# Performance work log

Hardware: AMD Instinct MI355X
Metric: run time of the kernel (lower is better)

## Reference

```python
import jax, jax.numpy as jnp
import numpy as np

E, K = 16, 4          # n_experts, top_k
C, H = 2048, 3584     # d_model, ffn_hidden
B, T = 2, 512
STD = 0.02


def setup_inputs() -> dict:
    key = jax.random.key(0)
    ks = jax.random.split(key, 5)
    x = jax.random.normal(ks[0], (B, T, C), jnp.float32)
    W_up = jax.random.normal(ks[1], (E, H, C), jnp.float32) * STD
    W_gate = jax.random.normal(ks[2], (E, H, C), jnp.float32) * STD
    W_down = jax.random.normal(ks[3], (E, C, H), jnp.float32) * STD
    gate_inp = jax.random.normal(ks[4], (E, C), jnp.float32) * STD
    return {"x": x, "W_up": W_up, "W_gate": W_gate, "W_down": W_down,
            "gate_inp": gate_inp}


def reference(x, W_up, W_gate, W_down, gate_inp):
    # x: [B, T, C]
    b, t, c = x.shape
    xf = x.reshape(b * t, c)                                  # [N, C]
    logits = xf @ gate_inp.T                                  # [N, E]
    topv, topi = jax.lax.top_k(logits, K)                     # [N, K]
    w = jax.nn.softmax(topv.astype(jnp.float32), axis=-1).astype(x.dtype)
    n = xf.shape[0]
    # Dense combine weights: zero for unselected experts -> identical math
    # to the original per-token gather, without the [N,K,H,C] blowup.
    dense_w = jnp.zeros((n, E), x.dtype).at[jnp.arange(n)[:, None], topi].set(w)
    u = jnp.einsum('nc,ehc->neh', xf, W_up)                   # [N, E, H]
    g = jnp.einsum('nc,ehc->neh', xf, W_gate)                 # [N, E, H]
    h = jax.nn.silu(g) * u                                    # SwiGLU
    y = jnp.einsum('neh,ech,ne->nc', h, W_down, dense_w)      # weighted combine
    return y.reshape(b, t, c)
```

## Files before the change

### kernel.cpp

```cpp
#include <hip/hip_runtime.h>
#include <math.h>

#define NTOK   1024
#define EXP    16
#define TOPK   4
#define DMODEL 2048
#define DFFN   3584
#define HT_TILES 56
#define CT_TILES 32
#define NSLOT  4096
#define MCH    128
#define NCHMAX 48

typedef __attribute__((ext_vector_type(8))) short bf16x8;
typedef __attribute__((ext_vector_type(4))) float f32x4;

#define O_COUNTS 0
#define O_BASE   256
#define O_CURSOR 512
#define O_CHT    1024
#define O_TOPI   4096
#define O_TOPW   (O_TOPI + 16384)
#define O_TOK    (O_TOPW + 16384)
#define O_WGT    (O_TOK + 16384)
#define O_SLOTNK (O_WGT + 16384)
#define O_XG     (O_SLOTNK + 16384)
#define O_HBUF   (O_XG + (size_t)NSLOT*DMODEL*2)

#define VMW(N) asm volatile("s_waitcnt vmcnt(" #N ")" ::: "memory")
#define LKW0() asm volatile("s_waitcnt lgkmcnt(0)" ::: "memory")
#define BAR()  __builtin_amdgcn_s_barrier()

__device__ __forceinline__ unsigned short f2b_rne(float f) {
  unsigned u = __builtin_bit_cast(unsigned, f);
  u += 0x7FFFu + ((u >> 16) & 1u);
  return (unsigned short)(u >> 16);
}
__device__ __forceinline__ float b2f(unsigned short h) {
  unsigned u = ((unsigned)h) << 16;
  return __builtin_bit_cast(float, u);
}
__device__ __forceinline__ unsigned pk2(float lo, float hi) {
  unsigned r;
  asm("v_cvt_pk_bf16_f32 %0, %1, %2" : "=v"(r) : "v"(lo), "v"(hi));
  return r;
}
__device__ __forceinline__ bf16x8 pack8(float4 a, float4 b) {
  union { unsigned u[4]; bf16x8 v; } r;
  r.u[0] = pk2(a.x, a.y); r.u[1] = pk2(a.z, a.w);
  r.u[2] = pk2(b.x, b.y); r.u[3] = pk2(b.z, b.w);
  return r.v;
}

__device__ __forceinline__ void gl16(const unsigned short* g, unsigned short* l) {
  __builtin_amdgcn_global_load_lds(
      (const __attribute__((address_space(1))) void*)g,
      (__attribute__((address_space(3))) void*)l, 16, 0, 0);
}

__device__ __forceinline__ bf16x8 ld_frag(const unsigned short* lds, int row, int chunk) {
  return *(const bf16x8*)(lds + row*64 + ((chunk ^ (row & 7)) * 8));
}

__global__ void k_zero(int* counts, int* cursor) {
  int t = threadIdx.x;
  if (t < EXP) { counts[t] = 0; cursor[t] = 0; }
}

__global__ void k_gate(const float* __restrict__ x, const float* __restrict__ gi,
                       int* __restrict__ topi, float* __restrict__ topw,
                       int* __restrict__ counts) {
  int n = blockIdx.x;
  int lane = threadIdx.x & 63, wave = threadIdx.x >> 6;
  __shared__ float lg[EXP];
  const float4* xr = (const float4*)(x + (size_t)n * DMODEL);
  #pragma unroll
  for (int i = 0; i < 4; ++i) {
    int e = wave * 4 + i;
    const float4* gr = (const float4*)(gi + (size_t)e * DMODEL);
    float s = 0.f;
    #pragma unroll
    for (int j = 0; j < 8; ++j) {
      float4 a = xr[j*64 + lane];
      float4 b = gr[j*64 + lane];
      s += a.x*b.x + a.y*b.y + a.z*b.z + a.w*b.w;
    }
    #pragma unroll
    for (int off = 32; off; off >>= 1) s += __shfl_xor(s, off);
    if (lane == 0) lg[e] = s;
  }
  __syncthreads();
  if (threadIdx.x == 0) {
    float v[EXP];
    #pragma unroll
    for (int j = 0; j < EXP; ++j) v[j] = lg[j];
    int bi[TOPK]; float bv[TOPK];
    #pragma unroll
    for (int k = 0; k < TOPK; ++k) {
      float best = -3.4e38f; int bidx = 0;
      for (int j = 0; j < EXP; ++j) if (v[j] > best) { best = v[j]; bidx = j; }
      bv[k] = best; bi[k] = bidx; v[bidx] = -3.4e38f;
    }
    float m = bv[0], ss = 0.f, w[TOPK];
    #pragma unroll
    for (int k = 0; k < TOPK; ++k) { w[k] = expf(bv[k] - m); ss += w[k]; }
    #pragma unroll
    for (int k = 0; k < TOPK; ++k) {
      topi[n*TOPK + k] = bi[k];
      topw[n*TOPK + k] = w[k] / ss;
      atomicAdd(&counts[bi[k]], 1);
    }
  }
}

__global__ void k_prefix(const int* __restrict__ counts, int* __restrict__ basep,
                         int* __restrict__ chtab) {
  if (threadIdx.x == 0) {
    int acc = 0;
    for (int e = 0; e < EXP; ++e) { basep[e] = acc; acc += counts[e]; }
    int c = 0;
    for (int e = 0; e < EXP; ++e) {
      int nm = (counts[e] + MCH - 1) / MCH;
      for (int m = 0; m < nm; ++m) { chtab[1 + c] = (e << 8) | m; ++c; }
    }
    chtab[0] = c;
    for (; c < NCHMAX; ++c) chtab[1 + c] = -1;
  }
}

__global__ void k_scatter(const int* __restrict__ topi, const float* __restrict__ topw,
                          const int* __restrict__ basep, int* __restrict__ cursor,
                          int* __restrict__ tok, float* __restrict__ wgt,
                          int* __restrict__ slotnk) {
  int n = blockIdx.x * blockDim.x + threadIdx.x;
  if (n >= NTOK) return;
  #pragma unroll
  for (int k = 0; k < TOPK; ++k) {
    int e = topi[n*TOPK + k];
    int pos = atomicAdd(&cursor[e], 1);
    int slot = basep[e] + pos;
    tok[slot] = n;
    wgt[slot] = topw[n*TOPK + k];
    slotnk[n*TOPK + k] = slot;
  }
}

__global__ void k_gather(const float* __restrict__ x, const int* __restrict__ tok,
                         unsigned short* __restrict__ xg) {
  int slot = blockIdx.x;
  int t = tok[slot];
  int c0 = threadIdx.x * 8;
  const float* src = x + (size_t)t * DMODEL + c0;
  float4 a = *(const float4*)(src);
  float4 b = *(const float4*)(src + 4);
  uint4 o = {pk2(a.x, a.y), pk2(a.z, a.w), pk2(b.x, b.y), pk2(b.z, b.w)};
  *(uint4*)(xg + (size_t)slot * DMODEL + c0) = o;
}

#define UG_STEP(PC, PN, KC, CUR) do {                                          \
    VMW(12);                                                                   \
    BAR();                                                                     \
    VMW(4);                                                                    \
    PN[0] = pack8(rw0, rw1); PN[1] = pack8(rw2, rw3);                          \
    PN[2] = pack8(rw4, rw5); PN[3] = pack8(rw6, rw7);                          \
    int kn_ = (KC) + 2; if (kn_ > DMODEL/64 - 1) kn_ = DMODEL/64 - 1;          \
    const float* pu_ = wu_row + kn_*64;                                        \
    const float* pg_ = wg_row + kn_*64;                                        \
    rw0 = *(const float4*)(pu_);      rw1 = *(const float4*)(pu_ + 4);         \
    rw2 = *(const float4*)(pu_ + 32); rw3 = *(const float4*)(pu_ + 36);        \
    rw4 = *(const float4*)(pg_);      rw5 = *(const float4*)(pg_ + 4);         \
    rw6 = *(const float4*)(pg_ + 32); rw7 = *(const float4*)(pg_ + 36);        \
    int wb_ = (CUR) + 2; if (wb_ >= 3) wb_ -= 3;                               \
    unsigned short* xw_ = xs + wb_*8192;                                       \
    _Pragma("unroll")                                                          \
    for (int i_ = 0; i_ < 4; ++i_)                                             \
      gl16(bx[i_] + kn_*64, xw_ + (i_*4 + wave)*8*64);                         \
    const unsigned short* xr_ = xs + (CUR)*8192;                               \
    __builtin_amdgcn_s_setprio(1);                                             \
    _Pragma("unroll")                                                          \
    for (int kk_ = 0; kk_ < 2; ++kk_) {                                        \
      int chunk_ = kk_*4 + (lane >> 4);                                        \
      _Pragma("unroll")                                                        \
      for (int t_ = 0; t_ < 8; ++t_) {                                         \
        bf16x8 a_ = ld_frag(xr_, t_*16 + col, chunk_);                         \
        ua[t_] = __builtin_amdgcn_mfma_f32_16x16x32_bf16(a_, PC[kk_],   ua[t_], 0, 0, 0); \
        ga[t_] = __builtin_amdgcn_mfma_f32_16x16x32_bf16(a_, PC[2+kk_], ga[t_], 0, 0, 0); \
      }                                                                        \
    }                                                                          \
    __builtin_amdgcn_s_setprio(0);                                             \
  } while (0)

__global__ __launch_bounds__(256, 3) void k_upgate(
    const unsigned short* __restrict__ xg,
    const float* __restrict__ Wu, const float* __restrict__ Wg,
    const int* __restrict__ counts, const int* __restrict__ basep,
    const int* __restrict__ chtab, const float* __restrict__ wgt,
    unsigned short* __restrict__ hbuf) {
  int bid = blockIdx.x;
  int lb  = (bid & 7) * (NCHMAX*HT_TILES/8) + (bid >> 3);
  int cid = lb / HT_TILES, ht = lb % HT_TILES;
  int ent = chtab[1 + cid];
  if (ent < 0) return;
  int e = ent >> 8, mch = ent & 255;
  int n_e = counts[e], base_e = basep[e], mstart = mch * MCH;

  __shared__ unsigned short xs[3*8192];
  __shared__ float swgt[MCH];

  int tid = threadIdx.x;
  int lane = tid & 63, wave = tid >> 6;
  int col = lane & 15;
  int kgrp = (lane >> 4) * 8;
  const float* wu_row = Wu + ((size_t)e * DFFN + (size_t)(ht*64 + wave*16 + col)) * DMODEL + kgrp;
  const float* wg_row = Wg + ((size_t)e * DFFN + (size_t)(ht*64 + wave*16 + col)) * DMODEL + kgrp;

  int xrow_lo = lane >> 3;
  int xpc     = lane & 7;
  int swz     = (xpc ^ xrow_lo) * 8;

  const unsigned short* bx[4];
  #pragma unroll
  for (int i = 0; i < 4; ++i) {
    int row = (i*4 + wave)*8 + xrow_lo;
    int slotr = base_e + mstart + row;
    if (slotr > NSLOT-1) slotr = NSLOT-1;
    bx[i] = xg + (size_t)slotr*DMODEL + swz;
  }

  if (tid < MCH) {
    int r = mstart + tid;
    swgt[tid] = (r < n_e) ? wgt[base_e + r] : 0.f;
  }
  LKW0();

  float4 rw0, rw1, rw2, rw3, rw4, rw5, rw6, rw7;
  bf16x8 pA[4], pB[4];

  rw0 = *(const float4*)(wu_row);      rw1 = *(const float4*)(wu_row + 4);
  rw2 = *(const float4*)(wu_row + 32); rw3 = *(const float4*)(wu_row + 36);
  rw4 = *(const float4*)(wg_row);      rw5 = *(const float4*)(wg_row + 4);
  rw6 = *(const float4*)(wg_row + 32); rw7 = *(const float4*)(wg_row + 36);
  #pragma unroll
  for (int i = 0; i < 4; ++i) gl16(bx[i],        xs        + (i*4 + wave)*8*64);
  #pragma unroll
  for (int i = 0; i < 4; ++i) gl16(bx[i] + 64,   xs + 8192 + (i*4 + wave)*8*64);
  VMW(8);
  pA[0] = pack8(rw0, rw1); pA[1] = pack8(rw2, rw3);
  pA[2] = pack8(rw4, rw5); pA[3] = pack8(rw6, rw7);
  rw0 = *(const float4*)(wu_row + 64);      rw1 = *(const float4*)(wu_row + 68);
  rw2 = *(const float4*)(wu_row + 96);      rw3 = *(const float4*)(wu_row + 100);
  rw4 = *(const float4*)(wg_row + 64);      rw5 = *(const float4*)(wg_row + 68);
  rw6 = *(const float4*)(wg_row + 96);      rw7 = *(const float4*)(wg_row + 100);

  f32x4 ua[8], ga[8];
  #pragma unroll
  for (int t = 0; t < 8; ++t) { f32x4 z = {0.f,0.f,0.f,0.f}; ua[t] = z; ga[t] = z; }

  int cur = 0;
  #pragma unroll 1
  for (int kc = 0; kc < DMODEL/64; kc += 2) {
    UG_STEP(pA, pB, kc, cur);     cur = (cur == 2) ? 0 : cur + 1;
    UG_STEP(pB, pA, kc + 1, cur); cur = (cur == 2) ? 0 : cur + 1;
  }

  #pragma unroll
  for (int t = 0; t < 8; ++t)
    #pragma unroll
    for (int r = 0; r < 4; ++r) {
      int ml = t*16 + (lane >> 4)*4 + r;
      if (mstart + ml < n_e) {
        float u = ua[t][r], g = ga[t][r];
        float hv = u * (g / (1.f + expf(-g))) * swgt[ml];
        int slot = base_e + mstart + ml;
        hbuf[(size_t)slot*DFFN + ht*64 + wave*16 + col] = f2b_rne(hv);
      }
    }
}

#define DN_STEP(PC, PN, KC, CUR) do {                                          \
    VMW(8);                                                                    \
    BAR();                                                                     \
    VMW(4);                                                                    \
    PN[0] = pack8(rw0, rw1); PN[1] = pack8(rw2, rw3);                          \
    int kn_ = (KC) + 2; if (kn_ > DFFN/64 - 1) kn_ = DFFN/64 - 1;              \
    const float* pd_ = wd_row + kn_*64;                                        \
    rw0 = *(const float4*)(pd_);      rw1 = *(const float4*)(pd_ + 4);         \
    rw2 = *(const float4*)(pd_ + 32); rw3 = *(const float4*)(pd_ + 36);        \
    int wb_ = (CUR) + 2; if (wb_ >= 3) wb_ -= 3;                               \
    unsigned short* xw_ = hs + wb_*8192;                                       \
    _Pragma("unroll")                                                          \
    for (int i_ = 0; i_ < 4; ++i_)                                             \
      gl16(bh[i_] + kn_*64, xw_ + (i_*4 + wave)*8*64);                         \
    const unsigned short* xr_ = hs + (CUR)*8192;                               \
    __builtin_amdgcn_s_setprio(1);                                             \
    _Pragma("unroll")                                                          \
    for (int kk_ = 0; kk_ < 2; ++kk_) {                                        \
      int chunk_ = kk_*4 + (lane >> 4);                                        \
      _Pragma("unroll")                                                        \
      for (int t_ = 0; t_ < 8; ++t_) {                                         \
        bf16x8 a_ = ld_frag(xr_, t_*16 + col, chunk_);                         \
        acc[t_] = __builtin_amdgcn_mfma_f32_16x16x32_bf16(a_, PC[kk_], acc[t_], 0, 0, 0); \
      }                                                                        \
    }                                                                          \
    __builtin_amdgcn_s_setprio(0);                                             \
  } while (0)

__global__ __launch_bounds__(256, 3) void k_down(
    const unsigned short* __restrict__ hbuf, const float* __restrict__ Wd,
    const int* __restrict__ counts, const int* __restrict__ basep,
    const int* __restrict__ chtab,
    unsigned short* __restrict__ ypart) {
  int bid = blockIdx.x;
  int lb  = (bid & 7) * (NCHMAX*CT_TILES/8) + (bid >> 3);
  int cid = lb / CT_TILES, ct = lb % CT_TILES;
  int ent = chtab[1 + cid];
  if (ent < 0) return;
  int e = ent >> 8, mch = ent & 255;
  int n_e = counts[e], base_e = basep[e], mstart = mch * MCH;

  __shared__ unsigned short hs[3*8192];

  int tid = threadIdx.x;
  int lane = tid & 63, wave = tid >> 6;
  int col = lane & 15;
  int kgrp = (lane >> 4) * 8;
  const float* wd_row = Wd + ((size_t)e * DMODEL + (size_t)(ct*64 + wave*16 + col)) * DFFN + kgrp;

  int xrow_lo = lane >> 3;
  int xpc     = lane & 7;
  int swz     = (xpc ^ xrow_lo) * 8;

  const unsigned short* bh[4];
  #pragma unroll
  for (int i = 0; i < 4; ++i) {
    int row = (i*4 + wave)*8 + xrow_lo;
    int slotr = base_e + mstart + row;
    if (slotr > NSLOT-1) slotr = NSLOT-1;
    bh[i] = hbuf + (size_t)slotr*DFFN + swz;
  }

  float4 rw0, rw1, rw2, rw3;
  bf16x8 pA[2], pB[2];

  rw0 = *(const float4*)(wd_row);      rw1 = *(const float4*)(wd_row + 4);
  rw2 = *(const float4*)(wd_row + 32); rw3 = *(const float4*)(wd_row + 36);
  #pragma unroll
  for (int i = 0; i < 4; ++i) gl16(bh[i],      hs        + (i*4 + wave)*8*64);
  #pragma unroll
  for (int i = 0; i < 4; ++i) gl16(bh[i] + 64, hs + 8192 + (i*4 + wave)*8*64);
  VMW(8);
  pA[0] = pack8(rw0, rw1); pA[1] = pack8(rw2, rw3);
  rw0 = *(const float4*)(wd_row + 64); rw1 = *(const float4*)(wd_row + 68);
  rw2 = *(const float4*)(wd_row + 96); rw3 = *(const float4*)(wd_row + 100);

  f32x4 acc[8];
  #pragma unroll
  for (int t = 0; t < 8; ++t) { f32x4 z = {0.f,0.f,0.f,0.f}; acc[t] = z; }

  int cur = 0;
  #pragma unroll 1
  for (int hc = 0; hc < DFFN/64; hc += 2) {
    DN_STEP(pA, pB, hc, cur);     cur = (cur == 2) ? 0 : cur + 1;
    DN_STEP(pB, pA, hc + 1, cur); cur = (cur == 2) ? 0 : cur + 1;
  }

  #pragma unroll
  for (int t = 0; t < 8; ++t)
    #pragma unroll
    for (int r = 0; r < 4; ++r) {
      int ml = t*16 + (lane >> 4)*4 + r;
      if (mstart + ml < n_e) {
        int slot = base_e + mstart + ml;
        ypart[(size_t)slot*DMODEL + ct*64 + wave*16 + col] = f2b_rne(acc[t][r]);
      }
    }
}

__global__ void k_combine(const unsigned short* __restrict__ ypart,
                          const int* __restrict__ slotnk, float* __restrict__ out) {
  int n = blockIdx.x, tid = threadIdx.x;
  int c0 = tid * 8;
  float acc[8] = {0.f,0.f,0.f,0.f,0.f,0.f,0.f,0.f};
  #pragma unroll
  for (int k = 0; k < TOPK; ++k) {
    int slot = slotnk[n*TOPK + k];
    uint4 v = *(const uint4*)(ypart + (size_t)slot*DMODEL + c0);
    const unsigned short* p = (const unsigned short*)&v;
    #pragma unroll
    for (int j = 0; j < 8; ++j) acc[j] += b2f(p[j]);
  }
  float4 o0 = {acc[0], acc[1], acc[2], acc[3]};
  float4 o1 = {acc[4], acc[5], acc[6], acc[7]};
  *(float4*)(out + (size_t)n*DMODEL + c0)     = o0;
  *(float4*)(out + (size_t)n*DMODEL + c0 + 4) = o1;
}

extern "C" void kernel_launch(void* const* d_in, const int* in_sizes, int n_in,
                              void* d_out, int out_size, void* d_ws, size_t ws_size,
                              hipStream_t stream) {
  const float* x     = (const float*)d_in[0];
  const float* W_up  = (const float*)d_in[1];
  const float* W_gt  = (const float*)d_in[2];
  const float* W_dn  = (const float*)d_in[3];
  const float* g_in  = (const float*)d_in[4];
  float* out = (float*)d_out;
  char* ws = (char*)d_ws;

  int*   counts = (int*)(ws + O_COUNTS);
  int*   basep  = (int*)(ws + O_BASE);
  int*   cursor = (int*)(ws + O_CURSOR);
  int*   chtab  = (int*)(ws + O_CHT);
  int*   topi   = (int*)(ws + O_TOPI);
  float* topw   = (float*)(ws + O_TOPW);
  int*   tok    = (int*)(ws + O_TOK);
  float* wgt    = (float*)(ws + O_WGT);
  int*   slotnk = (int*)(ws + O_SLOTNK);
  unsigned short* xg    = (unsigned short*)(ws + O_XG);
  unsigned short* hbuf  = (unsigned short*)(ws + O_HBUF);
  unsigned short* ypart = xg;

  k_zero   <<<1, 64, 0, stream>>>(counts, cursor);
  k_gate   <<<NTOK, 256, 0, stream>>>(x, g_in, topi, topw, counts);
  k_prefix <<<1, 64, 0, stream>>>(counts, basep, chtab);
  k_scatter<<<4, 256, 0, stream>>>(topi, topw, basep, cursor, tok, wgt, slotnk);
  k_gather <<<NSLOT, 256, 0, stream>>>(x, tok, xg);
  k_upgate <<<NCHMAX*HT_TILES, 256, 0, stream>>>(xg, W_up, W_gt, counts, basep, chtab, wgt, hbuf);
  k_down   <<<NCHMAX*CT_TILES, 256, 0, stream>>>(hbuf, W_dn, counts, basep, chtab, ypart);
  k_combine<<<NTOK, 256, 0, stream>>>(ypart, slotnk, out);
}
```

Baseline: 964.6 us.

## Switch MoE GEMM kernels to double-buffered LDS pipeline and expert-major block order

After: 998.4 us. 1.04x slower.

```diff
diff --git a/kernel.cpp b/kernel.cpp
--- a/kernel.cpp
+++ b/kernel.cpp
@@ -30,6 +30,7 @@
 #define VMW(N) asm volatile("s_waitcnt vmcnt(" #N ")" ::: "memory")
 #define LKW0() asm volatile("s_waitcnt lgkmcnt(0)" ::: "memory")
 #define BAR()  __builtin_amdgcn_s_barrier()
+#define SBAR() __builtin_amdgcn_sched_barrier(0)
 
 __device__ __forceinline__ unsigned short f2b_rne(float f) {
   unsigned u = __builtin_bit_cast(unsigned, f);
@@ -157,37 +158,38 @@
   *(uint4*)(xg + (size_t)slot * DMODEL + c0) = o;
 }
 
-#define UG_STEP(PC, PN, KC, CUR) do {                                          \
-    VMW(12);                                                                   \
+#define UG_STEP(XSC, XSN, RA, RB, PK, PKN, KC) do {                            \
     BAR();                                                                     \
-    VMW(4);                                                                    \
-    PN[0] = pack8(rw0, rw1); PN[1] = pack8(rw2, rw3);                          \
-    PN[2] = pack8(rw4, rw5); PN[3] = pack8(rw6, rw7);                          \
+    int kx_ = (KC) + 1; if (kx_ > DMODEL/64 - 1) kx_ = DMODEL/64 - 1;          \
+    _Pragma("unroll")                                                          \
+    for (int i_ = 0; i_ < 4; ++i_)                                             \
+      gl16(bx[i_] + kx_*64, (XSN) + (i_*4 + wave)*8*64);                       \
+    SBAR();                                                                    \
     int kn_ = (KC) + 2; if (kn_ > DMODEL/64 - 1) kn_ = DMODEL/64 - 1;          \
     const float* pu_ = wu_row + kn_*64;                                        \
     const float* pg_ = wg_row + kn_*64;                                        \
-    rw0 = *(const float4*)(pu_);      rw1 = *(const float4*)(pu_ + 4);         \
-    rw2 = *(const float4*)(pu_ + 32); rw3 = *(const float4*)(pu_ + 36);        \
-    rw4 = *(const float4*)(pg_);      rw5 = *(const float4*)(pg_ + 4);         \
-    rw6 = *(const float4*)(pg_ + 32); rw7 = *(const float4*)(pg_ + 36);        \
-    int wb_ = (CUR) + 2; if (wb_ >= 3) wb_ -= 3;                               \
-    unsigned short* xw_ = xs + wb_*8192;                                       \
-    _Pragma("unroll")                                                          \
-    for (int i_ = 0; i_ < 4; ++i_)                                             \
-      gl16(bx[i_] + kn_*64, xw_ + (i_*4 + wave)*8*64);                         \
-    const unsigned short* xr_ = xs + (CUR)*8192;                               \
+    RA[0] = *(const float4*)(pu_);      RA[1] = *(const float4*)(pu_ + 4);     \
+    RA[2] = *(const float4*)(pu_ + 32); RA[3] = *(const float4*)(pu_ + 36);    \
+    RA[4] = *(const float4*)(pg_);      RA[5] = *(const float4*)(pg_ + 4);     \
+    RA[6] = *(const float4*)(pg_ + 32); RA[7] = *(const float4*)(pg_ + 36);    \
+    SBAR();                                                                    \
+    VMW(20);                                                                   \
+    BAR();                                                                     \
     __builtin_amdgcn_s_setprio(1);                                             \
     _Pragma("unroll")                                                          \
     for (int kk_ = 0; kk_ < 2; ++kk_) {                                        \
       int chunk_ = kk_*4 + (lane >> 4);                                        \
       _Pragma("unroll")                                                        \
       for (int t_ = 0; t_ < 8; ++t_) {                                         \
-        bf16x8 a_ = ld_frag(xr_, t_*16 + col, chunk_);                         \
-        ua[t_] = __builtin_amdgcn_mfma_f32_16x16x32_bf16(a_, PC[kk_],   ua[t_], 0, 0, 0); \
-        ga[t_] = __builtin_amdgcn_mfma_f32_16x16x32_bf16(a_, PC[2+kk_], ga[t_], 0, 0, 0); \
+        bf16x8 a_ = ld_frag((XSC), t_*16 + col, chunk_);                       \
+        ua[t_] = __builtin_amdgcn_mfma_f32_16x16x32_bf16(a_, PK[kk_],   ua[t_], 0, 0, 0); \
+        ga[t_] = __builtin_amdgcn_mfma_f32_16x16x32_bf16(a_, PK[2+kk_], ga[t_], 0, 0, 0); \
       }                                                                        \
     }                                                                          \
     __builtin_amdgcn_s_setprio(0);                                             \
+    VMW(12);                                                                   \
+    PKN[0] = pack8(RB[0], RB[1]); PKN[1] = pack8(RB[2], RB[3]);                \
+    PKN[2] = pack8(RB[4], RB[5]); PKN[3] = pack8(RB[6], RB[7]);                \
   } while (0)
 
 __global__ __launch_bounds__(256, 3) void k_upgate(
@@ -198,13 +200,13 @@
     unsigned short* __restrict__ hbuf) {
   int bid = blockIdx.x;
   int lb  = (bid & 7) * (NCHMAX*HT_TILES/8) + (bid >> 3);
-  int cid = lb / HT_TILES, ht = lb % HT_TILES;
+  int cid = lb % NCHMAX, ht = lb / NCHMAX;
   int ent = chtab[1 + cid];
   if (ent < 0) return;
   int e = ent >> 8, mch = ent & 255;
   int n_e = counts[e], base_e = basep[e], mstart = mch * MCH;
 
-  __shared__ unsigned short xs[3*8192];
+  __shared__ unsigned short xs[2][128*64];
   __shared__ float swgt[MCH];
 
   int tid = threadIdx.x;
@@ -233,34 +235,34 @@
   }
   LKW0();
 
-  float4 rw0, rw1, rw2, rw3, rw4, rw5, rw6, rw7;
-  bf16x8 pA[4], pB[4];
-
-  rw0 = *(const float4*)(wu_row);      rw1 = *(const float4*)(wu_row + 4);
-  rw2 = *(const float4*)(wu_row + 32); rw3 = *(const float4*)(wu_row + 36);
-  rw4 = *(const float4*)(wg_row);      rw5 = *(const float4*)(wg_row + 4);
-  rw6 = *(const float4*)(wg_row + 32); rw7 = *(const float4*)(wg_row + 36);
-  #pragma unroll
-  for (int i = 0; i < 4; ++i) gl16(bx[i],        xs        + (i*4 + wave)*8*64);
-  #pragma unroll
-  for (int i = 0; i < 4; ++i) gl16(bx[i] + 64,   xs + 8192 + (i*4 + wave)*8*64);
-  VMW(8);
-  pA[0] = pack8(rw0, rw1); pA[1] = pack8(rw2, rw3);
-  pA[2] = pack8(rw4, rw5); pA[3] = pack8(rw6, rw7);
-  rw0 = *(const float4*)(wu_row + 64);      rw1 = *(const float4*)(wu_row + 68);
-  rw2 = *(const float4*)(wu_row + 96);      rw3 = *(const float4*)(wu_row + 100);
-  rw4 = *(const float4*)(wg_row + 64);      rw5 = *(const float4*)(wg_row + 68);
-  rw6 = *(const float4*)(wg_row + 96);      rw7 = *(const float4*)(wg_row + 100);
+  float4 ra[8], rb[8];
+  bf16x8 pkA[4], pkB[4];
+  #pragma unroll
+  for (int i = 0; i < 4; ++i)
+    gl16(bx[i], &xs[0][(i*4 + wave)*8*64]);
+  SBAR();
+  ra[0] = *(const float4*)(wu_row);      ra[1] = *(const float4*)(wu_row + 4);
+  ra[2] = *(const float4*)(wu_row + 32); ra[3] = *(const float4*)(wu_row + 36);
+  ra[4] = *(const float4*)(wg_row);      ra[5] = *(const float4*)(wg_row + 4);
+  ra[6] = *(const float4*)(wg_row + 32); ra[7] = *(const float4*)(wg_row + 36);
+  SBAR();
+  VMW(0);
+  pkA[0] = pack8(ra[0], ra[1]); pkA[1] = pack8(ra[2], ra[3]);
+  pkA[2] = pack8(ra[4], ra[5]); pkA[3] = pack8(ra[6], ra[7]);
+  rb[0] = *(const float4*)(wu_row + 64); rb[1] = *(const float4*)(wu_row + 68);
+  rb[2] = *(const float4*)(wu_row + 96); rb[3] = *(const float4*)(wu_row + 100);
+  rb[4] = *(const float4*)(wg_row + 64); rb[5] = *(const float4*)(wg_row + 68);
+  rb[6] = *(const float4*)(wg_row + 96); rb[7] = *(const float4*)(wg_row + 100);
+  SBAR();
 
   f32x4 ua[8], ga[8];
   #pragma unroll
   for (int t = 0; t < 8; ++t) { f32x4 z = {0.f,0.f,0.f,0.f}; ua[t] = z; ga[t] = z; }
 
-  int cur = 0;
   #pragma unroll 1
   for (int kc = 0; kc < DMODEL/64; kc += 2) {
-    UG_STEP(pA, pB, kc, cur);     cur = (cur == 2) ? 0 : cur + 1;
-    UG_STEP(pB, pA, kc + 1, cur); cur = (cur == 2) ? 0 : cur + 1;
+    UG_STEP(xs[0], xs[1], ra, rb, pkA, pkB, kc);
+    UG_STEP(xs[1], xs[0], rb, ra, pkB, pkA, kc + 1);
   }
 
   #pragma unroll
@@ -277,32 +279,33 @@
     }
 }
 
-#define DN_STEP(PC, PN, KC, CUR) do {                                          \
-    VMW(8);                                                                    \
+#define DN_STEP(XSC, XSN, RA, RB, PK, PKN, KC) do {                            \
     BAR();                                                                     \
-    VMW(4);                                                                    \
-    PN[0] = pack8(rw0, rw1); PN[1] = pack8(rw2, rw3);                          \
+    int kx_ = (KC) + 1; if (kx_ > DFFN/64 - 1) kx_ = DFFN/64 - 1;              \
+    _Pragma("unroll")                                                          \
+    for (int i_ = 0; i_ < 4; ++i_)                                             \
+      gl16(bh[i_] + kx_*64, (XSN) + (i_*4 + wave)*8*64);                       \
+    SBAR();                                                                    \
     int kn_ = (KC) + 2; if (kn_ > DFFN/64 - 1) kn_ = DFFN/64 - 1;              \
     const float* pd_ = wd_row + kn_*64;                                        \
-    rw0 = *(const float4*)(pd_);      rw1 = *(const float4*)(pd_ + 4);         \
-    rw2 = *(const float4*)(pd_ + 32); rw3 = *(const float4*)(pd_ + 36);        \
-    int wb_ = (CUR) + 2; if (wb_ >= 3) wb_ -= 3;                               \
-    unsigned short* xw_ = hs + wb_*8192;                                       \
-    _Pragma("unroll")                                                          \
-    for (int i_ = 0; i_ < 4; ++i_)                                             \
-      gl16(bh[i_] + kn_*64, xw_ + (i_*4 + wave)*8*64);                         \
-    const unsigned short* xr_ = hs + (CUR)*8192;                               \
+    RA[0] = *(const float4*)(pd_);      RA[1] = *(const float4*)(pd_ + 4);     \
+    RA[2] = *(const float4*)(pd_ + 32); RA[3] = *(const float4*)(pd_ + 36);    \
+    SBAR();                                                                    \
+    VMW(12);                                                                   \
+    BAR();                                                                     \
     __builtin_amdgcn_s_setprio(1);                                             \
     _Pragma("unroll")                                                          \
     for (int kk_ = 0; kk_ < 2; ++kk_) {                                        \
       int chunk_ = kk_*4 + (lane >> 4);                                        \
       _Pragma("unroll")                                                        \
       for (int t_ = 0; t_ < 8; ++t_) {                                         \
-        bf16x8 a_ = ld_frag(xr_, t_*16 + col, chunk_);                         \
-        acc[t_] = __builtin_amdgcn_mfma_f32_16x16x32_bf16(a_, PC[kk_], acc[t_], 0, 0, 0); \
+        bf16x8 a_ = ld_frag((XSC), t_*16 + col, chunk_);                       \
+        acc[t_] = __builtin_amdgcn_mfma_f32_16x16x32_bf16(a_, PK[kk_], acc[t_], 0, 0, 0); \
       }                                                                        \
     }                                                                          \
     __builtin_amdgcn_s_setprio(0);                                             \
+    VMW(8);                                                                    \
+    PKN[0] = pack8(RB[0], RB[1]); PKN[1] = pack8(RB[2], RB[3]);                \
   } while (0)
 
 __global__ __launch_bounds__(256, 3) void k_down(
@@ -312,13 +315,13 @@
     unsigned short* __restrict__ ypart) {
   int bid = blockIdx.x;
   int lb  = (bid & 7) * (NCHMAX*CT_TILES/8) + (bid >> 3);
-  int cid = lb / CT_TILES, ct = lb % CT_TILES;
+  int cid = lb % NCHMAX, ct = lb / NCHMAX;
   int ent = chtab[1 + cid];
   if (ent < 0) return;
   int e = ent >> 8, mch = ent & 255;
   int n_e = counts[e], base_e = basep[e], mstart = mch * MCH;
 
-  __shared__ unsigned short hs[3*8192];
+  __shared__ unsigned short hs[2][128*64];
 
   int tid = threadIdx.x;
   int lane = tid & 63, wave = tid >> 6;
@@ -339,29 +342,29 @@
     bh[i] = hbuf + (size_t)slotr*DFFN + swz;
   }
 
-  float4 rw0, rw1, rw2, rw3;
-  bf16x8 pA[2], pB[2];
-
-  rw0 = *(const float4*)(wd_row);      rw1 = *(const float4*)(wd_row + 4);
-  rw2 = *(const float4*)(wd_row + 32); rw3 = *(const float4*)(wd_row + 36);
-  #pragma unroll
-  for (int i = 0; i < 4; ++i) gl16(bh[i],      hs        + (i*4 + wave)*8*64);
-  #pragma unroll
-  for (int i = 0; i < 4; ++i) gl16(bh[i] + 64, hs + 8192 + (i*4 + wave)*8*64);
-  VMW(8);
-  pA[0] = pack8(rw0, rw1); pA[1] = pack8(rw2, rw3);
-  rw0 = *(const float4*)(wd_row + 64); rw1 = *(const float4*)(wd_row + 68);
-  rw2 = *(const float4*)(wd_row + 96); rw3 = *(const float4*)(wd_row + 100);
+  float4 ra[4], rb[4];
+  bf16x8 pkA[2], pkB[2];
+  #pragma unroll
+  for (int i = 0; i < 4; ++i)
+    gl16(bh[i], &hs[0][(i*4 + wave)*8*64]);
+  SBAR();
+  ra[0] = *(const float4*)(wd_row);      ra[1] = *(const float4*)(wd_row + 4);
+  ra[2] = *(const float4*)(wd_row + 32); ra[3] = *(const float4*)(wd_row + 36);
+  SBAR();
+  VMW(0);
+  pkA[0] = pack8(ra[0], ra[1]); pkA[1] = pack8(ra[2], ra[3]);
+  rb[0] = *(const float4*)(wd_row + 64); rb[1] = *(const float4*)(wd_row + 68);
+  rb[2] = *(const float4*)(wd_row + 96); rb[3] = *(const float4*)(wd_row + 100);
+  SBAR();
 
   f32x4 acc[8];
   #pragma unroll
   for (int t = 0; t < 8; ++t) { f32x4 z = {0.f,0.f,0.f,0.f}; acc[t] = z; }
 
-  int cur = 0;
   #pragma unroll 1
   for (int hc = 0; hc < DFFN/64; hc += 2) {
-    DN_STEP(pA, pB, hc, cur);     cur = (cur == 2) ? 0 : cur + 1;
-    DN_STEP(pB, pA, hc + 1, cur); cur = (cur == 2) ? 0 : cur + 1;
+    DN_STEP(hs[0], hs[1], ra, rb, pkA, pkB, hc);
+    DN_STEP(hs[1], hs[0], rb, ra, pkB, pkA, hc + 1);
   }
 
   #pragma unroll
```
